# Optimization experiments

Measured on AMD Instinct MI355X. Metric: run time of the kernel, lower is better.

Reference implementation:

```python
import jax, jax.numpy as jnp
import numpy as np
import math

B, S, KV, D, H = 4, 512, 4096, 1024, 16
HD = D // H  # head_dim = 64


def setup_inputs() -> dict:
    key = jax.random.key(0)
    ks = jax.random.split(key, 12)
    scale = 0.02
    return {
        "x": jax.random.normal(ks[0], (B, S, D), dtype=jnp.float32),
        "xa": jax.random.normal(ks[1], (B, KV, D), dtype=jnp.float32),
        "Wq": jax.random.normal(ks[2], (D, D), dtype=jnp.float32) * scale,
        "bq": jax.random.normal(ks[3], (D,), dtype=jnp.float32) * scale,
        "Wk": jax.random.normal(ks[4], (D, D), dtype=jnp.float32) * scale,  # key has no bias
        "Wv": jax.random.normal(ks[5], (D, D), dtype=jnp.float32) * scale,
        "bv": jax.random.normal(ks[6], (D,), dtype=jnp.float32) * scale,
        "Wo": jax.random.normal(ks[7], (D, D), dtype=jnp.float32) * scale,
        "bo": jax.random.normal(ks[8], (D,), dtype=jnp.float32) * scale,
        "cache_k": jnp.zeros((B, H, KV, HD), dtype=jnp.float32),
        "cache_v": jnp.zeros((B, H, KV, HD), dtype=jnp.float32),
    }


def reference(x, xa, Wq, bq, Wk, Wv, bv, Wo, bo, cache_k, cache_v):
    bsz, seq_len, _ = x.shape
    kv_len = xa.shape[1]
    # projections (torch nn.Linear convention: y = x @ W^T + b)
    q = (x @ Wq.T + bq).reshape(bsz, seq_len, H, HD).transpose(0, 2, 1, 3)   # [B,H,S,HD]
    k = (xa @ Wk.T).reshape(bsz, kv_len, H, HD).transpose(0, 2, 1, 3)        # [B,H,KV,HD]
    v = (xa @ Wv.T + bv).reshape(bsz, kv_len, H, HD).transpose(0, 2, 1, 3)   # [B,H,KV,HD]
    # prefill path: scatter k/v into positions [0, kv_len) of the cache
    updated_k = cache_k.at[:, :, :kv_len, :].set(k)
    updated_v = cache_v.at[:, :, :kv_len, :].set(v)
    # attention over full cache, fp32 softmax as in the original
    scores = jnp.einsum('bhqd,bhkd->bhqk', q, updated_k) / math.sqrt(HD)
    probs = jax.nn.softmax(scores.astype(jnp.float32), axis=-1).astype(q.dtype)
    attn = jnp.einsum('bhqk,bhkd->bhqd', probs, updated_v)                   # [B,H,S,HD]
    attn = attn.transpose(0, 2, 1, 3).reshape(bsz, seq_len, H * HD)
    out = attn @ Wo.T + bo
    return out, updated_k, updated_v
```

## Files before the change

### kernel.cpp

```cpp
#include <hip/hip_runtime.h>
#include <hip/hip_bf16.h>

using u16 = unsigned short;
typedef __bf16 bf16x8 __attribute__((ext_vector_type(8)));
typedef float f32x4 __attribute__((ext_vector_type(4)));

#define SB 4
#define SS 512
#define SKV 4096
#define SD 1024
#define SH 16
#define SHD 64
#define NSPLIT 4
#define NROWS 32768
#define QSCALE 0.18033688011112042f
#define DEFER_THR 6.0f

__device__ inline u16 f2bf(float f){
  __hip_bfloat16 h = __float2bfloat16(f);
  return __builtin_bit_cast(u16, h);
}
__device__ inline float bf2f(u16 u){
  return __builtin_bit_cast(float, (unsigned)u << 16);
}

__device__ inline bf16x8 ld_frag_g(const u16* p){
  uint4 v = *reinterpret_cast<const uint4*>(p);
  return __builtin_bit_cast(bf16x8, v);
}

__device__ inline bf16x8 ld_frag_lds(const char* base, int ob){
  uint4 v = *reinterpret_cast<const uint4*>(base + ob);
  return __builtin_bit_cast(bf16x8, v);
}

__device__ inline unsigned pack_bf_trunc(float a, float b){
  return __builtin_amdgcn_perm(__builtin_bit_cast(unsigned, b),
                               __builtin_bit_cast(unsigned, a), 0x07060302u);
}

__global__ __launch_bounds__(256) void cast_kernel(const float* __restrict__ src,
                                                   u16* __restrict__ dst, int n4){
  int i = blockIdx.x * 256 + threadIdx.x;
  if (i < n4){
    float4 f = reinterpret_cast<const float4*>(src)[i];
    ushort4 u;
    u.x = f2bf(f.x); u.y = f2bf(f.y); u.z = f2bf(f.z); u.w = f2bf(f.w);
    reinterpret_cast<ushort4*>(dst)[i] = u;
  }
}

__global__ __launch_bounds__(256) void cast_w4(const float* __restrict__ s0,
                                               const float* __restrict__ s1,
                                               const float* __restrict__ s2,
                                               const float* __restrict__ s3,
                                               u16* __restrict__ dst){
  int which = blockIdx.x >> 10;
  int j = (blockIdx.x & 1023) * 256 + threadIdx.x;
  const float* s = which == 0 ? s0 : which == 1 ? s1 : which == 2 ? s2 : s3;
  float4 f = reinterpret_cast<const float4*>(s)[j];
  ushort4 u;
  u.x = f2bf(f.x); u.y = f2bf(f.y); u.z = f2bf(f.z); u.w = f2bf(f.w);
  reinterpret_cast<ushort4*>(dst + (long)which * 1048576L)[j] = u;
}

enum { MODE_Q = 0, MODE_K = 1, MODE_V = 2, MODE_OUT = 3 };

template<int MODE>
__global__ __launch_bounds__(256) void gemm_bt(const u16* __restrict__ A,
                                               const u16* __restrict__ W,
                                               const float* __restrict__ bias,
                                               float* __restrict__ outF,
                                               u16* __restrict__ outB)
{
  __shared__ u16 As[2][128*64];
  __shared__ u16 Bs[2][128*64];
  const int tid  = threadIdx.x;
  const int lane = tid & 63;
  const int wm   = ((tid >> 6) >> 1) * 64;
  const int wn   = ((tid >> 6) & 1) * 64;
  const long rowBase = (long)blockIdx.x * 128;
  const long colBase = (long)blockIdx.y * 128;

  f32x4 acc[4][4];
#pragma unroll
  for (int i = 0; i < 4; i++)
#pragma unroll
    for (int j = 0; j < 4; j++)
      acc[i][j] = (f32x4){0.f, 0.f, 0.f, 0.f};

  uint4 va[4], vw[4];
#pragma unroll
  for (int i = 0; i < 4; i++){
    int u = tid + i * 256;
    int r = u >> 3, c = u & 7;
    va[i] = *reinterpret_cast<const uint4*>(A + (rowBase + r) * 1024 + c * 8);
    vw[i] = *reinterpret_cast<const uint4*>(W + (colBase + r) * 1024 + c * 8);
  }
#pragma unroll
  for (int i = 0; i < 4; i++){
    int u = tid + i * 256;
    int r = u >> 3, c = u & 7;
    int ob = (r * 128 + c * 16) ^ ((r & 7) << 4);
    *reinterpret_cast<uint4*>(reinterpret_cast<char*>(As[0]) + ob) = va[i];
    *reinterpret_cast<uint4*>(reinterpret_cast<char*>(Bs[0]) + ob) = vw[i];
  }
  __syncthreads();

  int cur = 0;
  for (int kt = 0; kt < 16; ++kt){
    uint4 va2[4], vw2[4];
    if (kt < 15){
#pragma unroll
      for (int i = 0; i < 4; i++){
        int u = tid + i * 256;
        int r = u >> 3, c = u & 7;
        va2[i] = *reinterpret_cast<const uint4*>(A + (rowBase + r) * 1024 + (kt + 1) * 64 + c * 8);
        vw2[i] = *reinterpret_cast<const uint4*>(W + (colBase + r) * 1024 + (kt + 1) * 64 + c * 8);
      }
    }
    const char* ach = reinterpret_cast<const char*>(As[cur]);
    const char* bch = reinterpret_cast<const char*>(Bs[cur]);
#pragma unroll
    for (int kk = 0; kk < 2; kk++){
      bf16x8 af[4], bfr[4];
#pragma unroll
      for (int mi = 0; mi < 4; mi++){
        int row = wm + mi * 16 + (lane & 15);
        int ob = (row * 128 + kk * 64 + (lane >> 4) * 16) ^ ((row & 7) << 4);
        af[mi] = ld_frag_lds(ach, ob);
      }
#pragma unroll
      for (int ni = 0; ni < 4; ni++){
        int row = wn + ni * 16 + (lane & 15);
        int ob = (row * 128 + kk * 64 + (lane >> 4) * 16) ^ ((row & 7) << 4);
        bfr[ni] = ld_frag_lds(bch, ob);
      }
#pragma unroll
      for (int mi = 0; mi < 4; mi++)
#pragma unroll
        for (int ni = 0; ni < 4; ni++)
          acc[mi][ni] = __builtin_amdgcn_mfma_f32_16x16x32_bf16(af[mi], bfr[ni], acc[mi][ni], 0, 0, 0);
    }
    if (kt < 15){
#pragma unroll
      for (int i = 0; i < 4; i++){
        int u = tid + i * 256;
        int r = u >> 3, c = u & 7;
        int ob = (r * 128 + c * 16) ^ ((r & 7) << 4);
        *reinterpret_cast<uint4*>(reinterpret_cast<char*>(As[cur ^ 1]) + ob) = va2[i];
        *reinterpret_cast<uint4*>(reinterpret_cast<char*>(Bs[cur ^ 1]) + ob) = vw2[i];
      }
      __syncthreads();
    }
    cur ^= 1;
  }

#pragma unroll
  for (int mi = 0; mi < 4; mi++){
#pragma unroll
    for (int ni = 0; ni < 4; ni++){
      long gn = colBase + wn + ni * 16 + (lane & 15);
      float bb = bias[gn];
#pragma unroll
      for (int r = 0; r < 4; r++){
        long gm = rowBase + wm + mi * 16 + ((lane >> 4) << 2) + r;
        float val = acc[mi][ni][r] + bb;
        if (MODE == MODE_OUT){
          outF[gm * 1024 + gn] = val;
        } else {
          long b = gm >> 9, s = gm & 511;
          long h = gn >> 6, hd = gn & 63;
          outB[((b * SH + h) * SS + s) * SHD + hd] = f2bf(val * QSCALE);
        }
      }
    }
  }
}

template<int MODE>
__global__ __launch_bounds__(512) void gemm_bt256(const u16* __restrict__ A,
                                                  const u16* __restrict__ W,
                                                  const float* __restrict__ bias,
                                                  float* __restrict__ outF,
                                                  u16* __restrict__ outB)
{
  __shared__ u16 As[2][256*64];
  __shared__ u16 Bs[2][256*64];
  const int tid  = threadIdx.x;
  const int lane = tid & 63;
  const int wid  = tid >> 6;
  const int wm   = (wid >> 2) * 128;
  const int wn   = (wid & 3) * 64;
  int lin = blockIdx.x;
  int xcd = lin & 7, j = lin >> 3;
  const long rowBase = (long)(xcd * 8 + (j >> 2)) * 256;
  const long colBase = (long)(j & 3) * 256;

  f32x4 acc[8][4];
#pragma unroll
  for (int i = 0; i < 8; i++)
#pragma unroll
    for (int jj = 0; jj < 4; jj++)
      acc[i][jj] = (f32x4){0.f, 0.f, 0.f, 0.f};

  uint4 va[4], vw[4];
#pragma unroll
  for (int i = 0; i < 4; i++){
    int u = tid + i * 512;
    int r = u >> 3, c = u & 7;
    va[i] = *reinterpret_cast<const uint4*>(A + (rowBase + r) * 1024 + c * 8);
    vw[i] = *reinterpret_cast<const uint4*>(W + (colBase + r) * 1024 + c * 8);
  }
#pragma unroll
  for (int i = 0; i < 4; i++){
    int u = tid + i * 512;
    int r = u >> 3, c = u & 7;
    int ob = (r * 128 + c * 16) ^ ((r & 7) << 4);
    *reinterpret_cast<uint4*>(reinterpret_cast<char*>(As[0]) + ob) = va[i];
    *reinterpret_cast<uint4*>(reinterpret_cast<char*>(Bs[0]) + ob) = vw[i];
  }
  __syncthreads();

  int cur = 0;
  for (int kt = 0; kt < 16; ++kt){
    uint4 va2[4], vw2[4];
    if (kt < 15){
#pragma unroll
      for (int i = 0; i < 4; i++){
        int u = tid + i * 512;
        int r = u >> 3, c = u & 7;
        va2[i] = *reinterpret_cast<const uint4*>(A + (rowBase + r) * 1024 + (kt + 1) * 64 + c * 8);
        vw2[i] = *reinterpret_cast<const uint4*>(W + (colBase + r) * 1024 + (kt + 1) * 64 + c * 8);
      }
    }
    const char* ach = reinterpret_cast<const char*>(As[cur]);
    const char* bch = reinterpret_cast<const char*>(Bs[cur]);
#pragma unroll
    for (int kk = 0; kk < 2; kk++){
      bf16x8 af[8], bfr[4];
#pragma unroll
      for (int mi = 0; mi < 8; mi++){
        int row = wm + mi * 16 + (lane & 15);
        int ob = (row * 128 + kk * 64 + (lane >> 4) * 16) ^ ((row & 7) << 4);
        af[mi] = ld_frag_lds(ach, ob);
      }
#pragma unroll
      for (int ni = 0; ni < 4; ni++){
        int row = wn + ni * 16 + (lane & 15);
        int ob = (row * 128 + kk * 64 + (lane >> 4) * 16) ^ ((row & 7) << 4);
        bfr[ni] = ld_frag_lds(bch, ob);
      }
#pragma unroll
      for (int mi = 0; mi < 8; mi++)
#pragma unroll
        for (int ni = 0; ni < 4; ni++)
          acc[mi][ni] = __builtin_amdgcn_mfma_f32_16x16x32_bf16(af[mi], bfr[ni], acc[mi][ni], 0, 0, 0);
    }
    if (kt < 15){
#pragma unroll
      for (int i = 0; i < 4; i++){
        int u = tid + i * 512;
        int r = u >> 3, c = u & 7;
        int ob = (r * 128 + c * 16) ^ ((r & 7) << 4);
        *reinterpret_cast<uint4*>(reinterpret_cast<char*>(As[cur ^ 1]) + ob) = va2[i];
        *reinterpret_cast<uint4*>(reinterpret_cast<char*>(Bs[cur ^ 1]) + ob) = vw2[i];
      }
      __syncthreads();
    }
    cur ^= 1;
  }

#pragma unroll
  for (int mi = 0; mi < 8; mi++){
#pragma unroll
    for (int ni = 0; ni < 4; ni++){
      long gn = colBase + wn + ni * 16 + (lane & 15);
      long h = gn >> 6, hd = gn & 63;
      if (MODE == MODE_V){
        float bb = bias[gn];
        long gmBase = rowBase + wm + mi * 16 + ((lane >> 4) << 2);
        long b = gmBase >> 12, kv = gmBase & 4095;
        long fidx = ((b * SH + h) * SKV + kv) * SHD + hd;
        ushort4 pk;
        float v0 = acc[mi][ni][0] + bb; outF[fidx          ] = v0; pk.x = f2bf(v0);
        float v1 = acc[mi][ni][1] + bb; outF[fidx +     SHD] = v1; pk.y = f2bf(v1);
        float v2 = acc[mi][ni][2] + bb; outF[fidx + 2 * SHD] = v2; pk.z = f2bf(v2);
        float v3 = acc[mi][ni][3] + bb; outF[fidx + 3 * SHD] = v3; pk.w = f2bf(v3);
        *reinterpret_cast<ushort4*>(outB + ((b * SH + h) * SHD + hd) * SKV + kv) = pk;
      } else {
#pragma unroll
        for (int r = 0; r < 4; r++){
          long gm = rowBase + wm + mi * 16 + ((lane >> 4) << 2) + r;
          long b = gm >> 12, kv = gm & 4095;
          long idx = ((b * SH + h) * SKV + kv) * SHD + hd;
          float val = acc[mi][ni][r];
          outF[idx] = val;
          outB[idx] = f2bf(val);
        }
      }
    }
  }
}

__global__ __launch_bounds__(512) void attn_partial(const u16* __restrict__ qb,
                                                    const u16* __restrict__ kb,
                                                    const u16* __restrict__ vTb,
                                                    u16* __restrict__ opartB,
                                                    float* __restrict__ ml){
  __shared__ u16 Klds[2][64 * 64];
  __shared__ u16 Vlds[2][64 * 64];
  __shared__ u16 PT[8][16 * 72];
  const int tid  = threadIdx.x;
  const int lane = tid & 63;
  const int wid  = tid >> 6;
  const int c    = lane & 15;
  const int hi   = lane >> 4;
  const long bh  = blockIdx.x;
  const int  qt  = blockIdx.y;
  const int  split = blockIdx.z;

  const u16* qp = qb + (bh * SS + qt * 128 + wid * 16 + c) * SHD + hi * 8;
  const bf16x8 bq0 = ld_frag_g(qp);
  const bf16x8 bq1 = ld_frag_g(qp + 32);

  f32x4 acc[4];
#pragma unroll
  for (int i = 0; i < 4; i++) acc[i] = (f32x4){0.f, 0.f, 0.f, 0.f};
  float mrun = -INFINITY;
  f32x4 lrunv = (f32x4){0.f, 0.f, 0.f, 0.f};

  const u16* kbase = kb  + bh * SKV * SHD;
  const u16* vbase = vTb + bh * SHD * SKV;
  u16* pt = &PT[wid][0];
  const int sr  = tid >> 3;
  const int scc = tid & 7;
  const int sob = (sr * 128 + scc * 16) ^ ((sr & 7) << 4);
  const int t0 = split * 16;

  {
    uint4 kv4 = *reinterpret_cast<const uint4*>(kbase + (t0 * 64 + sr) * SHD + scc * 8);
    uint4 vv4 = *reinterpret_cast<const uint4*>(vbase + (long)sr * SKV + t0 * 64 + scc * 8);
    *reinterpret_cast<uint4*>(reinterpret_cast<char*>(Klds[0]) + sob) = kv4;
    *reinterpret_cast<uint4*>(reinterpret_cast<char*>(Vlds[0]) + sob) = vv4;
  }
  __syncthreads();

  int cur = 0;
  for (int kt = t0; kt < t0 + 16; ++kt){
    const bool hn = kt + 1 < t0 + 16;
    uint4 kn, vn;
    if (hn){
      kn = *reinterpret_cast<const uint4*>(kbase + ((kt + 1) * 64 + sr) * SHD + scc * 8);
      vn = *reinterpret_cast<const uint4*>(vbase + (long)sr * SKV + (kt + 1) * 64 + scc * 8);
    }
    const char* kch = reinterpret_cast<const char*>(Klds[cur]);
    const char* vch = reinterpret_cast<const char*>(Vlds[cur]);

    f32x4 sT[4];
#pragma unroll
    for (int ni = 0; ni < 4; ni++){
      int krow = ni * 16 + c;
      int swz = (krow & 7) << 4;
      int a0 = (krow * 128 + hi * 16) ^ swz;
      int a1 = (krow * 128 + 64 + hi * 16) ^ swz;
      f32x4 z = (f32x4){0.f, 0.f, 0.f, 0.f};
      sT[ni] = __builtin_amdgcn_mfma_f32_16x16x32_bf16(ld_frag_lds(kch, a0), bq0, z, 0, 0, 0);
      sT[ni] = __builtin_amdgcn_mfma_f32_16x16x32_bf16(ld_frag_lds(kch, a1), bq1, sT[ni], 0, 0, 0);
    }
    f32x4 mv = __builtin_elementwise_max(__builtin_elementwise_max(sT[0], sT[1]),
                                         __builtin_elementwise_max(sT[2], sT[3]));
    float t = fmaxf(fmaxf(mv[0], mv[1]), fmaxf(mv[2], mv[3]));
    if (!__all(t <= mrun + DEFER_THR)){
      float tr = fmaxf(t, __shfl_xor(t, 16));
      tr = fmaxf(tr, __shfl_xor(tr, 32));
      float mn = fmaxf(mrun, tr);
      float al = exp2f(mrun - mn);
      lrunv *= al;
#pragma unroll
      for (int ni = 0; ni < 4; ni++) acc[ni] *= al;
      mrun = mn;
    }
#pragma unroll
    for (int ni = 0; ni < 4; ni++){
      f32x4 p;
      p[0] = exp2f(sT[ni][0] - mrun); p[1] = exp2f(sT[ni][1] - mrun);
      p[2] = exp2f(sT[ni][2] - mrun); p[3] = exp2f(sT[ni][3] - mrun);
      lrunv += p;
      unsigned lo = pack_bf_trunc(p[0], p[1]);
      unsigned hp = pack_bf_trunc(p[2], p[3]);
      uint2 w; w.x = lo; w.y = hp;
      *reinterpret_cast<uint2*>(pt + c * 72 + ni * 16 + hi * 4) = w;
    }
#pragma unroll
    for (int m = 0; m < 2; m++){
      bf16x8 pfrag = __builtin_bit_cast(bf16x8,
          *reinterpret_cast<const uint4*>(pt + c * 72 + m * 32 + hi * 8));
#pragma unroll
      for (int ni = 0; ni < 4; ni++){
        int vrow = ni * 16 + c;
        int av = (vrow * 128 + m * 64 + hi * 16) ^ ((vrow & 7) << 4);
        acc[ni] = __builtin_amdgcn_mfma_f32_16x16x32_bf16(ld_frag_lds(vch, av), pfrag, acc[ni], 0, 0, 0);
      }
    }
    if (hn){
      *reinterpret_cast<uint4*>(reinterpret_cast<char*>(Klds[cur ^ 1]) + sob) = kn;
      *reinterpret_cast<uint4*>(reinterpret_cast<char*>(Vlds[cur ^ 1]) + sob) = vn;
      __syncthreads();
    }
    cur ^= 1;
  }

  float l = (lrunv[0] + lrunv[1]) + (lrunv[2] + lrunv[3]);
  l += __shfl_xor(l, 16);
  l += __shfl_xor(l, 32);
  const long row = bh * SS + (long)qt * 128 + wid * 16 + c;
  u16* ob = opartB + ((long)split * NROWS + row) * SHD;
#pragma unroll
  for (int ni = 0; ni < 4; ni++){
    ushort4 pk;
    pk.x = f2bf(acc[ni][0]); pk.y = f2bf(acc[ni][1]);
    pk.z = f2bf(acc[ni][2]); pk.w = f2bf(acc[ni][3]);
    *reinterpret_cast<ushort4*>(ob + ni * 16 + hi * 4) = pk;
  }
  if (hi == 0){
    ml[(long)split * NROWS + row] = mrun;
    ml[(long)NSPLIT * NROWS + (long)split * NROWS + row] = l;
  }
}

__global__ __launch_bounds__(256) void attn_combine(const u16* __restrict__ opartB,
                                                    const float* __restrict__ ml,
                                                    u16* __restrict__ attnb){
  long idx4 = (long)blockIdx.x * 256 + threadIdx.x;
  long row = idx4 >> 4;
  int  c   = (int)(idx4 & 15);
  float m0 = ml[row], m1 = ml[NROWS + row], m2 = ml[2L*NROWS + row], m3 = ml[3L*NROWS + row];
  float M = fmaxf(fmaxf(m0, m1), fmaxf(m2, m3));
  float w0 = exp2f(m0 - M), w1 = exp2f(m1 - M), w2 = exp2f(m2 - M), w3 = exp2f(m3 - M);
  const float* lb = ml + (long)NSPLIT * NROWS;
  float L = w0*lb[row] + w1*lb[NROWS+row] + w2*lb[2L*NROWS+row] + w3*lb[3L*NROWS+row];
  float inv = 1.f / L;
  const ushort4* op = reinterpret_cast<const ushort4*>(opartB);
  ushort4 v0 = op[(0L*NROWS + row) * 16 + c];
  ushort4 v1 = op[(1L*NROWS + row) * 16 + c];
  ushort4 v2 = op[(2L*NROWS + row) * 16 + c];
  ushort4 v3 = op[(3L*NROWS + row) * 16 + c];
  float4 val;
  val.x = (w0*bf2f(v0.x) + w1*bf2f(v1.x) + w2*bf2f(v2.x) + w3*bf2f(v3.x)) * inv;
  val.y = (w0*bf2f(v0.y) + w1*bf2f(v1.y) + w2*bf2f(v2.y) + w3*bf2f(v3.y)) * inv;
  val.z = (w0*bf2f(v0.z) + w1*bf2f(v1.z) + w2*bf2f(v2.z) + w3*bf2f(v3.z)) * inv;
  val.w = (w0*bf2f(v0.w) + w1*bf2f(v1.w) + w2*bf2f(v2.w) + w3*bf2f(v3.w)) * inv;
  long bh = row >> 9, s = row & 511;
  long b = bh >> 4, h = bh & 15;
  ushort4 u;
  u.x = f2bf(val.x); u.y = f2bf(val.y); u.z = f2bf(val.z); u.w = f2bf(val.w);
  reinterpret_cast<ushort4*>(attnb)[((b * SS + s) * SD + h * SHD) / 4 + c] = u;
}

extern "C" void kernel_launch(void* const* d_in, const int* in_sizes, int n_in,
                              void* d_out, int out_size, void* d_ws, size_t ws_size,
                              hipStream_t stream)
{
  const float* x  = (const float*)d_in[0];
  const float* xa = (const float*)d_in[1];
  const float* Wq = (const float*)d_in[2];
  const float* bq = (const float*)d_in[3];
  const float* Wk = (const float*)d_in[4];
  const float* Wv = (const float*)d_in[5];
  const float* bv = (const float*)d_in[6];
  const float* Wo = (const float*)d_in[7];
  const float* bo = (const float*)d_in[8];

  float* outO = (float*)d_out;
  float* outK = outO + (long)SB * SS * SD;
  float* outV = outK + (long)SB * SH * SKV * SHD;

  u16* ws   = (u16*)d_ws;
  u16* xb   = ws;
  u16* xab  = xb   + 2097152L;
  u16* Wqb  = xab  + 16777216L;
  u16* Wkb  = Wqb  + 1048576L;
  u16* Wvb  = Wkb  + 1048576L;
  u16* Wob  = Wvb  + 1048576L;
  u16* qbuf = Wob  + 1048576L;
  u16* kbuf = qbuf + 2097152L;
  u16* vTbuf= kbuf + 16777216L;
  u16* mlb  = vTbuf+ 16777216L;

  u16*   attnb  = xb;
  u16*   opartB = xab;
  float* ml     = (float*)mlb;

  cast_kernel<<<2048, 256, 0, stream>>>(x,  xb,  524288);
  cast_kernel<<<16384, 256, 0, stream>>>(xa, xab, 4194304);
  cast_w4    <<<4096, 256, 0, stream>>>(Wq, Wk, Wv, Wo, Wqb);

  gemm_bt<MODE_Q>     <<<dim3(16, 8), 256, 0, stream>>>(xb,  Wqb, bq, nullptr, qbuf);
  gemm_bt256<MODE_K>  <<<256,         512, 0, stream>>>(xab, Wkb, nullptr, outK, kbuf);
  gemm_bt256<MODE_V>  <<<256,         512, 0, stream>>>(xab, Wvb, bv, outV, vTbuf);
  attn_partial        <<<dim3(64, 4, NSPLIT), 512, 0, stream>>>(qbuf, kbuf, vTbuf, opartB, ml);
  attn_combine        <<<2048, 256, 0, stream>>>(opartB, ml, attnb);
  gemm_bt<MODE_OUT>   <<<dim3(16, 8), 256, 0, stream>>>(attnb, Wob, bo, outO, nullptr);
}
```

Baseline: 254.3 us.

## Fuse xa fp32-to-bf16 cast into merged K/V projection GEMM

Removes the separate cast pass over xa and has the K/V GEMM load fp32 xa directly, converting to bf16 on the fly. K and V projections are merged into one launch with 128x128 tiles over 2048 blocks, a role bit picking K or V. This drops a 64MB read and 32MB write of xa and one kernel launch. In exchange each GEMM tile re-reads fp32 xa, which is twice the bytes, and converts it repeatedly across column tiles. The smaller tiles also lower data reuse per block.

```diff
diff --git a/kernel.cpp b/kernel.cpp
--- a/kernel.cpp
+++ b/kernel.cpp
@@ -37,6 +37,20 @@
 __device__ inline unsigned pack_bf_trunc(float a, float b){
   return __builtin_amdgcn_perm(__builtin_bit_cast(unsigned, b),
                                __builtin_bit_cast(unsigned, a), 0x07060302u);
+}
+
+__device__ inline uint4 ld_cvt8(const float* p){
+  float4 f0 = *reinterpret_cast<const float4*>(p);
+  float4 f1 = *reinterpret_cast<const float4*>(p + 4);
+  ushort4 a, b;
+  a.x = f2bf(f0.x); a.y = f2bf(f0.y); a.z = f2bf(f0.z); a.w = f2bf(f0.w);
+  b.x = f2bf(f1.x); b.y = f2bf(f1.y); b.z = f2bf(f1.z); b.w = f2bf(f1.w);
+  uint4 r;
+  r.x = (unsigned)a.x | ((unsigned)a.y << 16);
+  r.y = (unsigned)a.z | ((unsigned)a.w << 16);
+  r.z = (unsigned)b.x | ((unsigned)b.y << 16);
+  r.w = (unsigned)b.z | ((unsigned)b.w << 16);
+  return r;
 }
 
 __global__ __launch_bounds__(256) void cast_kernel(const float* __restrict__ src,
@@ -178,28 +192,32 @@
   }
 }
 
-template<int MODE>
-__global__ __launch_bounds__(512) void gemm_bt256(const u16* __restrict__ A,
-                                                  const u16* __restrict__ W,
-                                                  const float* __restrict__ bias,
-                                                  float* __restrict__ outF,
-                                                  u16* __restrict__ outB)
+__global__ __launch_bounds__(256) void gemm_kv(const float* __restrict__ Axa,
+                                               const u16* __restrict__ Wkb,
+                                               const u16* __restrict__ Wvb,
+                                               const float* __restrict__ bv,
+                                               float* __restrict__ outK,
+                                               u16* __restrict__ outKb,
+                                               float* __restrict__ outV,
+                                               u16* __restrict__ outVTb)
 {
-  __shared__ u16 As[2][256*64];
-  __shared__ u16 Bs[2][256*64];
+  __shared__ u16 As[2][128*64];
+  __shared__ u16 Bs[2][128*64];
   const int tid  = threadIdx.x;
   const int lane = tid & 63;
-  const int wid  = tid >> 6;
-  const int wm   = (wid >> 2) * 128;
-  const int wn   = (wid & 3) * 64;
-  int lin = blockIdx.x;
-  int xcd = lin & 7, j = lin >> 3;
-  const long rowBase = (long)(xcd * 8 + (j >> 2)) * 256;
-  const long colBase = (long)(j & 3) * 256;
-
-  f32x4 acc[8][4];
-#pragma unroll
-  for (int i = 0; i < 8; i++)
+  const int wm   = ((tid >> 6) >> 1) * 64;
+  const int wn   = ((tid >> 6) & 1) * 64;
+  const int lin  = blockIdx.x;
+  const int xcd  = lin & 7;
+  const int role = (lin >> 3) & 1;
+  const int j    = lin >> 4;
+  const long rowBase = (long)(xcd * 16 + (j >> 3)) * 128;
+  const long colBase = (long)(j & 7) * 128;
+  const u16* W = role ? Wvb : Wkb;
+
+  f32x4 acc[4][4];
+#pragma unroll
+  for (int i = 0; i < 4; i++)
 #pragma unroll
     for (int jj = 0; jj < 4; jj++)
       acc[i][jj] = (f32x4){0.f, 0.f, 0.f, 0.f};
@@ -207,14 +225,14 @@
   uint4 va[4], vw[4];
 #pragma unroll
   for (int i = 0; i < 4; i++){
-    int u = tid + i * 512;
+    int u = tid + i * 256;
     int r = u >> 3, c = u & 7;
-    va[i] = *reinterpret_cast<const uint4*>(A + (rowBase + r) * 1024 + c * 8);
+    va[i] = ld_cvt8(Axa + (rowBase + r) * 1024 + c * 8);
     vw[i] = *reinterpret_cast<const uint4*>(W + (colBase + r) * 1024 + c * 8);
   }
 #pragma unroll
   for (int i = 0; i < 4; i++){
-    int u = tid + i * 512;
+    int u = tid + i * 256;
     int r = u >> 3, c = u & 7;
     int ob = (r * 128 + c * 16) ^ ((r & 7) << 4);
     *reinterpret_cast<uint4*>(reinterpret_cast<char*>(As[0]) + ob) = va[i];
@@ -228,9 +246,9 @@
     if (kt < 15){
 #pragma unroll
       for (int i = 0; i < 4; i++){
-        int u = tid + i * 512;
+        int u = tid + i * 256;
         int r = u >> 3, c = u & 7;
-        va2[i] = *reinterpret_cast<const uint4*>(A + (rowBase + r) * 1024 + (kt + 1) * 64 + c * 8);
+        va2[i] = ld_cvt8(Axa + (rowBase + r) * 1024 + (kt + 1) * 64 + c * 8);
         vw2[i] = *reinterpret_cast<const uint4*>(W + (colBase + r) * 1024 + (kt + 1) * 64 + c * 8);
       }
     }
@@ -238,9 +256,9 @@
     const char* bch = reinterpret_cast<const char*>(Bs[cur]);
 #pragma unroll
     for (int kk = 0; kk < 2; kk++){
-      bf16x8 af[8], bfr[4];
-#pragma unroll
-      for (int mi = 0; mi < 8; mi++){
+      bf16x8 af[4], bfr[4];
+#pragma unroll
+      for (int mi = 0; mi < 4; mi++){
         int row = wm + mi * 16 + (lane & 15);
         int ob = (row * 128 + kk * 64 + (lane >> 4) * 16) ^ ((row & 7) << 4);
         af[mi] = ld_frag_lds(ach, ob);
@@ -252,7 +270,7 @@
         bfr[ni] = ld_frag_lds(bch, ob);
       }
 #pragma unroll
-      for (int mi = 0; mi < 8; mi++)
+      for (int mi = 0; mi < 4; mi++)
 #pragma unroll
         for (int ni = 0; ni < 4; ni++)
           acc[mi][ni] = __builtin_amdgcn_mfma_f32_16x16x32_bf16(af[mi], bfr[ni], acc[mi][ni], 0, 0, 0);
@@ -260,7 +278,7 @@
     if (kt < 15){
 #pragma unroll
       for (int i = 0; i < 4; i++){
-        int u = tid + i * 512;
+        int u = tid + i * 256;
         int r = u >> 3, c = u & 7;
         int ob = (r * 128 + c * 16) ^ ((r & 7) << 4);
         *reinterpret_cast<uint4*>(reinterpret_cast<char*>(As[cur ^ 1]) + ob) = va2[i];
@@ -272,22 +290,22 @@
   }
 
 #pragma unroll
-  for (int mi = 0; mi < 8; mi++){
+  for (int mi = 0; mi < 4; mi++){
 #pragma unroll
     for (int ni = 0; ni < 4; ni++){
       long gn = colBase + wn + ni * 16 + (lane & 15);
       long h = gn >> 6, hd = gn & 63;
-      if (MODE == MODE_V){
-        float bb = bias[gn];
+      if (role){
+        float bb = bv[gn];
         long gmBase = rowBase + wm + mi * 16 + ((lane >> 4) << 2);
         long b = gmBase >> 12, kv = gmBase & 4095;
         long fidx = ((b * SH + h) * SKV + kv) * SHD + hd;
         ushort4 pk;
-        float v0 = acc[mi][ni][0] + bb; outF[fidx          ] = v0; pk.x = f2bf(v0);
-        float v1 = acc[mi][ni][1] + bb; outF[fidx +     SHD] = v1; pk.y = f2bf(v1);
-        float v2 = acc[mi][ni][2] + bb; outF[fidx + 2 * SHD] = v2; pk.z = f2bf(v2);
-        float v3 = acc[mi][ni][3] + bb; outF[fidx + 3 * SHD] = v3; pk.w = f2bf(v3);
-        *reinterpret_cast<ushort4*>(outB + ((b * SH + h) * SHD + hd) * SKV + kv) = pk;
+        float v0 = acc[mi][ni][0] + bb; outV[fidx          ] = v0; pk.x = f2bf(v0);
+        float v1 = acc[mi][ni][1] + bb; outV[fidx +     SHD] = v1; pk.y = f2bf(v1);
+        float v2 = acc[mi][ni][2] + bb; outV[fidx + 2 * SHD] = v2; pk.z = f2bf(v2);
+        float v3 = acc[mi][ni][3] + bb; outV[fidx + 3 * SHD] = v3; pk.w = f2bf(v3);
+        *reinterpret_cast<ushort4*>(outVTb + ((b * SH + h) * SHD + hd) * SKV + kv) = pk;
       } else {
 #pragma unroll
         for (int r = 0; r < 4; r++){
@@ -295,8 +313,8 @@
           long b = gm >> 12, kv = gm & 4095;
           long idx = ((b * SH + h) * SKV + kv) * SHD + hd;
           float val = acc[mi][ni][r];
-          outF[idx] = val;
-          outB[idx] = f2bf(val);
+          outK[idx] = val;
+          outKb[idx] = f2bf(val);
         }
       }
     }
@@ -493,13 +511,12 @@
   float* ml     = (float*)mlb;
 
   cast_kernel<<<2048, 256, 0, stream>>>(x,  xb,  524288);
-  cast_kernel<<<16384, 256, 0, stream>>>(xa, xab, 4194304);
   cast_w4    <<<4096, 256, 0, stream>>>(Wq, Wk, Wv, Wo, Wqb);
 
-  gemm_bt<MODE_Q>     <<<dim3(16, 8), 256, 0, stream>>>(xb,  Wqb, bq, nullptr, qbuf);
-  gemm_bt256<MODE_K>  <<<256,         512, 0, stream>>>(xab, Wkb, nullptr, outK, kbuf);
-  gemm_bt256<MODE_V>  <<<256,         512, 0, stream>>>(xab, Wvb, bv, outV, vTbuf);
-  attn_partial        <<<dim3(64, 4, NSPLIT), 512, 0, stream>>>(qbuf, kbuf, vTbuf, opartB, ml);
-  attn_combine        <<<2048, 256, 0, stream>>>(opartB, ml, attnb);
-  gemm_bt<MODE_OUT>   <<<dim3(16, 8), 256, 0, stream>>>(attnb, Wob, bo, outO, nullptr);
-}
+  gemm_bt<MODE_Q>   <<<dim3(16, 8), 256, 0, stream>>>(xb,  Wqb, bq, nullptr, qbuf);
+  gemm_kv           <<<2048,        256, 0, stream>>>(xa, Wkb, Wvb, bv,
+                                                      outK, kbuf, outV, vTbuf);
+  attn_partial      <<<dim3(64, 4, NSPLIT), 512, 0, stream>>>(qbuf, kbuf, vTbuf, opartB, ml);
+  attn_combine      <<<2048, 256, 0, stream>>>(opartB, ml, attnb);
+  gemm_bt<MODE_OUT> <<<dim3(16, 8), 256, 0, stream>>>(attnb, Wob, bo, outO, nullptr);
+}
```

Result: slower. 295.3 us (+16.1%).
